# Optimization experiments

Hardware: AMD Instinct MI355X
Metric: run time of the kernel (lower is better)

Reference implementation:

```python
import jax, jax.numpy as jnp
import numpy as np

N = 100000


def gcn_conv(x, edge_index, W, b):
    """PyG GCNConv: add self-loops, symmetric normalization, x @ W, aggregate, + bias."""
    n = x.shape[0]
    src = jnp.concatenate([edge_index[0], jnp.arange(n)])
    dst = jnp.concatenate([edge_index[1], jnp.arange(n)])
    deg = jax.ops.segment_sum(jnp.ones_like(dst, dtype=x.dtype), dst, num_segments=n)
    dinv = jnp.where(deg > 0, jax.lax.rsqrt(deg), 0.0)
    norm = dinv[src] * dinv[dst]  # [E+N]
    h = x @ W  # [N, out]
    msg = h[src] * norm[:, None]  # gather + scale
    agg = jax.ops.segment_sum(msg, dst, num_segments=n)
    return agg + b


def setup_inputs() -> dict:
    key = jax.random.key(0)
    ks = jax.random.split(key, 10)
    x = jax.random.normal(ks[0], (N, 256), dtype=jnp.float32)
    edge_index = jax.random.randint(ks[1], (2, 3200000), 0, N, dtype=jnp.int64)
    def glorot(k, fan_in, fan_out):
        s = np.sqrt(6.0 / (fan_in + fan_out)).astype(np.float32)
        return jax.random.uniform(k, (fan_in, fan_out), jnp.float32, -s, s)
    return {
        "x": x,
        "edge_index": edge_index,
        "W1": glorot(ks[2], 256, 128), "b1": jnp.zeros((128,), jnp.float32),
        "W2": glorot(ks[3], 128, 64), "b2": jnp.zeros((64,), jnp.float32),
        "W3": glorot(ks[4], 64, 16), "b3": jnp.zeros((16,), jnp.float32),
        "Wc": glorot(ks[5], 16, 2), "bc": jnp.zeros((2,), jnp.float32),
    }


def reference(x, edge_index, W1, b1, W2, b2, W3, b3, Wc, bc):
    h = jnp.tanh(gcn_conv(x, edge_index, W1, b1))
    h = jnp.tanh(gcn_conv(h, edge_index, W2, b2))
    h = jnp.tanh(gcn_conv(h, edge_index, W3, b3))
    out = h @ Wc + bc
    return (out, h)
```

## Files before the change

kernel.cpp:

```cpp
#include <hip/hip_runtime.h>
#include <hip/hip_fp16.h>
#include <cstdint>
#include <cstddef>


#define EPB 16384
#define BSHIFT 8
#define NBUC_MAX 512
#define BCAP 12800

__global__ __launch_bounds__(256) void scan_block(const int* __restrict__ src, int n,
                                                  int* __restrict__ incl,
                                                  int* __restrict__ bsum) {
    int tid = threadIdx.x;
    int v = blockIdx.x * 256 + tid;
    int val = (v < n) ? src[v] : 0;
    int lane = tid & 63, w = tid >> 6;
#pragma unroll
    for (int off = 1; off < 64; off <<= 1) {
        int t = __shfl_up(val, off, 64);
        if (lane >= off) val += t;
    }
    __shared__ int wsum[4];
    if (lane == 63) wsum[w] = val;
    __syncthreads();
#pragma unroll
    for (int i = 0; i < 4; ++i)
        if (i < w) val += wsum[i];
    if (v < n) incl[v] = val;
    if (tid == 255) bsum[blockIdx.x] = val;
}

__global__ __launch_bounds__(512) void scan_sums(int* __restrict__ bsum, int nb) {
    int tid = threadIdx.x;
    int val = (tid < nb) ? bsum[tid] : 0;
    int lane = tid & 63, w = tid >> 6;
#pragma unroll
    for (int off = 1; off < 64; off <<= 1) {
        int t = __shfl_up(val, off, 64);
        if (lane >= off) val += t;
    }
    __shared__ int wsum[8];
    if (lane == 63) wsum[w] = val;
    __syncthreads();
#pragma unroll
    for (int i = 0; i < 8; ++i)
        if (i < w) val += wsum[i];
    if (tid < nb) bsum[tid] = val;
}

__global__ __launch_bounds__(256) void finalize_scan(
    const int* __restrict__ incl, const int* __restrict__ bsum,
    const int* __restrict__ src, int n, int* __restrict__ excl) {
    int v = blockIdx.x * 256 + threadIdx.x;
    if (v >= n) return;
    int boff = (blockIdx.x == 0) ? 0 : bsum[blockIdx.x - 1];
    excl[v] = boff + incl[v] - src[v];
}

__global__ __launch_bounds__(256) void hist_bucket(
    const int* __restrict__ ei, int E, int nbuc, int nch,
    int* __restrict__ histG) {
    __shared__ int h[NBUC_MAX];
    const int k = blockIdx.x;
    for (int b = threadIdx.x; b < NBUC_MAX; b += 256) h[b] = 0;
    __syncthreads();
    const int base = k * EPB, end = min(E, base + EPB);
    for (int i = base + threadIdx.x; i < end; i += 256)
        atomicAdd(&h[ei[(size_t)E + i] >> BSHIFT], 1);
    __syncthreads();
    for (int b = threadIdx.x; b < nbuc; b += 256)
        histG[(size_t)b * nch + k] = h[b];
}

__global__ __launch_bounds__(256) void bucket_scatter(
    const int* __restrict__ ei, int E, int nbuc, int nch,
    const int* __restrict__ offs, uint2* __restrict__ ebuf) {
    __shared__ int cur[NBUC_MAX];
    const int k = blockIdx.x;
    for (int b = threadIdx.x; b < nbuc; b += 256)
        cur[b] = offs[(size_t)b * nch + k];
    __syncthreads();
    const int base = k * EPB, end = min(E, base + EPB);
    for (int i = base + threadIdx.x; i < end; i += 256) {
        int s = ei[i];
        int d = ei[(size_t)E + i];
        int pos = atomicAdd(&cur[d >> BSHIFT], 1);
        ebuf[pos] = make_uint2((unsigned)s, (unsigned)d);
    }
}

__global__ __launch_bounds__(256) void bucket_build(
    const uint2* __restrict__ ebuf, const int* __restrict__ offs,
    int E, int nbuc, int nch, int n,
    int* __restrict__ col, int* __restrict__ deg,
    int* __restrict__ row_start, float* __restrict__ dinv) {
    const int b = blockIdx.x;
    const int tid = threadIdx.x;
    const int estart = offs[(size_t)b * nch];
    const int eend = (b + 1 < nbuc) ? offs[(size_t)(b + 1) * nch] : E;
    const int cnt = eend - estart;

    __shared__ int degl[256];
    __shared__ int curl[256];
    __shared__ int wsum[4];
    __shared__ int colstage[BCAP];

    degl[tid] = 0;
    __syncthreads();
    for (int i = tid; i < cnt; i += 256)
        atomicAdd(&degl[ebuf[estart + i].y & 255], 1);
    __syncthreads();
    int myDeg = degl[tid];
    int val = myDeg;
    int lane = tid & 63, w = tid >> 6;
#pragma unroll
    for (int off = 1; off < 64; off <<= 1) {
        int t = __shfl_up(val, off, 64);
        if (lane >= off) val += t;
    }
    if (lane == 63) wsum[w] = val;
    __syncthreads();
#pragma unroll
    for (int i = 0; i < 4; ++i)
        if (i < w) val += wsum[i];
    int excl = val - myDeg;
    curl[tid] = excl;
    int v = (b << BSHIFT) + tid;
    if (v < n) {
        deg[v] = myDeg;
        row_start[v] = estart + excl;
        dinv[v] = rsqrtf((float)(myDeg + 1));
    }
    __syncthreads();
    if (cnt <= BCAP) {
        for (int i = tid; i < cnt; i += 256) {
            uint2 e = ebuf[estart + i];
            int pos = atomicAdd(&curl[e.y & 255], 1);
            colstage[pos] = (int)e.x;
        }
        __syncthreads();
        for (int i = tid; i < cnt; i += 256)
            col[estart + i] = colstage[i];
    } else {
        for (int i = tid; i < cnt; i += 256) {
            uint2 e = ebuf[estart + i];
            int pos = atomicAdd(&curl[e.y & 255], 1);
            col[estart + pos] = (int)e.x;
        }
    }
}

__device__ inline unsigned int pack2h(float a, float b) {
    __half ha = __float2half_rn(a), hb = __float2half_rn(b);
    unsigned short ua = *(unsigned short*)&ha, ub = *(unsigned short*)&hb;
    return (unsigned int)ua | ((unsigned int)ub << 16);
}

template <int FIN, int FOUT, int TM>
__global__ __launch_bounds__(256) void gemm_tile_h(
    const float* __restrict__ X, const float* __restrict__ W,
    const float* __restrict__ dinv, __half* __restrict__ Hs, int n) {
    constexpr int CT = FOUT / 4;
    constexpr int RG = 256 / CT;
    static_assert(TM == RG * 4, "tile mismatch");
    constexpr int LROW = FIN + 4;
    __shared__ float xs[TM][LROW];

    const int node0 = blockIdx.x * TM;
    const int tid = threadIdx.x;

    constexpr int C4 = FIN / 4;
    for (int i = tid; i < TM * C4; i += 256) {
        int r = i / C4, c = i % C4;
        float4 v = make_float4(0.f, 0.f, 0.f, 0.f);
        if (node0 + r < n) v = *(const float4*)(X + (size_t)(node0 + r) * FIN + c * 4);
        *(float4*)&xs[r][c * 4] = v;
    }
    __syncthreads();

    const int col = (tid % CT) * 4;
    const int r0 = (tid / CT) * 4;

    float acc[4][4];
#pragma unroll
    for (int i = 0; i < 4; ++i)
#pragma unroll
        for (int j = 0; j < 4; ++j) acc[i][j] = 0.f;

#pragma unroll 2
    for (int k = 0; k < FIN; k += 4) {
        float4 w0 = *(const float4*)(W + (size_t)(k + 0) * FOUT + col);
        float4 w1 = *(const float4*)(W + (size_t)(k + 1) * FOUT + col);
        float4 w2 = *(const float4*)(W + (size_t)(k + 2) * FOUT + col);
        float4 w3 = *(const float4*)(W + (size_t)(k + 3) * FOUT + col);
        float4 av[4];
        av[0] = *(const float4*)&xs[r0 + 0][k];
        av[1] = *(const float4*)&xs[r0 + 1][k];
        av[2] = *(const float4*)&xs[r0 + 2][k];
        av[3] = *(const float4*)&xs[r0 + 3][k];
#pragma unroll
        for (int rr = 0; rr < 4; ++rr) {
            acc[rr][0] = fmaf(av[rr].x, w0.x, acc[rr][0]);
            acc[rr][1] = fmaf(av[rr].x, w0.y, acc[rr][1]);
            acc[rr][2] = fmaf(av[rr].x, w0.z, acc[rr][2]);
            acc[rr][3] = fmaf(av[rr].x, w0.w, acc[rr][3]);
            acc[rr][0] = fmaf(av[rr].y, w1.x, acc[rr][0]);
            acc[rr][1] = fmaf(av[rr].y, w1.y, acc[rr][1]);
            acc[rr][2] = fmaf(av[rr].y, w1.z, acc[rr][2]);
            acc[rr][3] = fmaf(av[rr].y, w1.w, acc[rr][3]);
            acc[rr][0] = fmaf(av[rr].z, w2.x, acc[rr][0]);
            acc[rr][1] = fmaf(av[rr].z, w2.y, acc[rr][1]);
            acc[rr][2] = fmaf(av[rr].z, w2.z, acc[rr][2]);
            acc[rr][3] = fmaf(av[rr].z, w2.w, acc[rr][3]);
            acc[rr][0] = fmaf(av[rr].w, w3.x, acc[rr][0]);
            acc[rr][1] = fmaf(av[rr].w, w3.y, acc[rr][1]);
            acc[rr][2] = fmaf(av[rr].w, w3.z, acc[rr][2]);
            acc[rr][3] = fmaf(av[rr].w, w3.w, acc[rr][3]);
        }
    }

#pragma unroll
    for (int rr = 0; rr < 4; ++rr) {
        int node = node0 + r0 + rr;
        if (node < n) {
            float di = dinv[node];
            uint2 pk;
            pk.x = pack2h(acc[rr][0] * di, acc[rr][1] * di);
            pk.y = pack2h(acc[rr][2] * di, acc[rr][3] * di);
            *(uint2*)(Hs + (size_t)node * FOUT + col) = pk;
        }
    }
}

__device__ inline void add8h(float* acc, uint4 p) {
    unsigned int w[4] = {p.x, p.y, p.z, p.w};
#pragma unroll
    for (int t = 0; t < 4; ++t) {
        __half2 h = *(const __half2*)&w[t];
        float2 f = __half22float2(h);
        acc[2 * t] += f.x;
        acc[2 * t + 1] += f.y;
    }
}

template <int F>
__global__ __launch_bounds__(256) void pull_agg_h(
    const int* __restrict__ row_start, const int* __restrict__ deg,
    const int* __restrict__ col, const __half* __restrict__ Hs,
    const float* __restrict__ dinv, const float* __restrict__ B,
    float* __restrict__ OUT, int n) {
    constexpr int TPE = F / 8;
    long long gid = (long long)blockIdx.x * 256 + threadIdx.x;
    int node = (int)(gid / TPE);
    int lane = (int)(gid % TPE);
    if (node >= n) return;
    const int beg = row_start[node];
    const int cnt = deg[node];
    const size_t lo = (size_t)lane * 8;

    float acc[8] = {0.f, 0.f, 0.f, 0.f, 0.f, 0.f, 0.f, 0.f};
    add8h(acc, *(const uint4*)(Hs + (size_t)node * F + lo));

    int j = 0;
    for (; j + 8 <= cnt; j += 8) {
        int s0 = col[beg + j + 0], s1 = col[beg + j + 1];
        int s2 = col[beg + j + 2], s3 = col[beg + j + 3];
        int s4 = col[beg + j + 4], s5 = col[beg + j + 5];
        int s6 = col[beg + j + 6], s7 = col[beg + j + 7];
        uint4 p0 = *(const uint4*)(Hs + (size_t)s0 * F + lo);
        uint4 p1 = *(const uint4*)(Hs + (size_t)s1 * F + lo);
        uint4 p2 = *(const uint4*)(Hs + (size_t)s2 * F + lo);
        uint4 p3 = *(const uint4*)(Hs + (size_t)s3 * F + lo);
        uint4 p4 = *(const uint4*)(Hs + (size_t)s4 * F + lo);
        uint4 p5 = *(const uint4*)(Hs + (size_t)s5 * F + lo);
        uint4 p6 = *(const uint4*)(Hs + (size_t)s6 * F + lo);
        uint4 p7 = *(const uint4*)(Hs + (size_t)s7 * F + lo);
        add8h(acc, p0); add8h(acc, p1); add8h(acc, p2); add8h(acc, p3);
        add8h(acc, p4); add8h(acc, p5); add8h(acc, p6); add8h(acc, p7);
    }
    for (; j < cnt; ++j) {
        int s = col[beg + j];
        add8h(acc, *(const uint4*)(Hs + (size_t)s * F + lo));
    }

    float di = dinv[node];
    float4 b0 = *(const float4*)(B + lo);
    float4 b1 = *(const float4*)(B + lo + 4);
    float4 r0, r1;
    r0.x = tanhf(fmaf(acc[0], di, b0.x));
    r0.y = tanhf(fmaf(acc[1], di, b0.y));
    r0.z = tanhf(fmaf(acc[2], di, b0.z));
    r0.w = tanhf(fmaf(acc[3], di, b0.w));
    r1.x = tanhf(fmaf(acc[4], di, b1.x));
    r1.y = tanhf(fmaf(acc[5], di, b1.y));
    r1.z = tanhf(fmaf(acc[6], di, b1.z));
    r1.w = tanhf(fmaf(acc[7], di, b1.w));
    float* op = OUT + (size_t)node * F + lo;
    *(float4*)(op) = r0;
    *(float4*)(op + 4) = r1;
}

__global__ void classifier_kernel(const float* __restrict__ Hf,
                                  const float* __restrict__ Wc,
                                  const float* __restrict__ bc,
                                  float* __restrict__ out, int n) {
    int v = blockIdx.x * blockDim.x + threadIdx.x;
    if (v >= n) return;
    float o0 = bc[0], o1 = bc[1];
    const float* h = Hf + (size_t)v * 16;
#pragma unroll
    for (int k = 0; k < 16; ++k) {
        float hv = h[k];
        o0 = fmaf(hv, Wc[k * 2 + 0], o0);
        o1 = fmaf(hv, Wc[k * 2 + 1], o1);
    }
    out[(size_t)v * 2 + 0] = o0;
    out[(size_t)v * 2 + 1] = o1;
}

extern "C" void kernel_launch(void* const* d_in, const int* in_sizes, int n_in,
                              void* d_out, int out_size, void* d_ws, size_t ws_size,
                              hipStream_t stream) {
    const float* x  = (const float*)d_in[0];
    const int* ei   = (const int*)d_in[1];
    const float* W1 = (const float*)d_in[2];
    const float* b1 = (const float*)d_in[3];
    const float* W2 = (const float*)d_in[4];
    const float* b2 = (const float*)d_in[5];
    const float* W3 = (const float*)d_in[6];
    const float* b3 = (const float*)d_in[7];
    const float* Wc = (const float*)d_in[8];
    const float* bc = (const float*)d_in[9];

    const int n = in_sizes[0] / 256;
    const int E = in_sizes[1] / 2;
    const int nbuc = (n + 255) >> BSHIFT;
    const int nch  = (E + EPB - 1) / EPB;
    const int NH   = nbuc * nch;
    const int nb2  = (NH + 255) / 256;

    float* outp = (float*)d_out;
    float* outh = outp + (size_t)n * 2;

    int*    deg       = (int*)d_ws;
    float*  dinv      = (float*)d_ws + (size_t)n;
    int*    row_start = (int*)d_ws + 2 * (size_t)n;
    int*    histG     = (int*)d_ws + 3 * (size_t)n;
    int*    incl      = histG + NH;
    int*    bsum      = incl + NH;
    int*    offs      = bsum + 512;
    int*    col       = offs + NH;
    __half* HsH       = (__half*)(col + E);
    float*  xbuf      = (float*)(HsH + (size_t)n * 128);
    uint2*  ebuf      = (uint2*)xbuf;

    hist_bucket<<<nch, 256, 0, stream>>>(ei, E, nbuc, nch, histG);
    scan_block<<<nb2, 256, 0, stream>>>(histG, NH, incl, bsum);
    scan_sums<<<1, 512, 0, stream>>>(bsum, nb2);
    finalize_scan<<<nb2, 256, 0, stream>>>(incl, bsum, histG, NH, offs);
    bucket_scatter<<<nch, 256, 0, stream>>>(ei, E, nbuc, nch, offs, ebuf);
    bucket_build<<<nbuc, 256, 0, stream>>>(ebuf, offs, E, nbuc, nch, n,
                                           col, deg, row_start, dinv);

    gemm_tile_h<256, 128, 32><<<(n + 31) / 32, 256, 0, stream>>>(x, W1, dinv, HsH, n);
    pull_agg_h<128><<<(int)(((long long)n * 16 + 255) / 256), 256, 0, stream>>>(
        row_start, deg, col, HsH, dinv, b1, xbuf, n);

    gemm_tile_h<128, 64, 64><<<(n + 63) / 64, 256, 0, stream>>>(xbuf, W2, dinv, HsH, n);
    pull_agg_h<64><<<(int)(((long long)n * 8 + 255) / 256), 256, 0, stream>>>(
        row_start, deg, col, HsH, dinv, b2, xbuf, n);

    gemm_tile_h<64, 16, 256><<<(n + 255) / 256, 256, 0, stream>>>(xbuf, W3, dinv, HsH, n);
    pull_agg_h<16><<<(int)(((long long)n * 2 + 255) / 256), 256, 0, stream>>>(
        row_start, deg, col, HsH, dinv, b3, outh, n);

    classifier_kernel<<<(n + 255) / 256, 256, 0, stream>>>(outh, Wc, bc, outp, n);
}
```

Baseline: 713.8 us.

## Use bf16x3 split MFMA for the first two GCN layer GEMMs

Replaces the FP32 shared-memory tiled GEMMs for layers 1 and 2 with MFMA-based kernels. Each operand is split into a bf16 high part and a bf16 residual, and three bf16 products are summed to recover near-FP32 accuracy. The weights are pre-packed each call into the lane layout that MFMA expects, and the packed copies reuse the histogram workspace. This targets the ALU cost of the dense GEMMs, at the price of extra pack launches and some accuracy risk.

```diff
diff --git a/kernel.cpp b/kernel.cpp
--- a/kernel.cpp
+++ b/kernel.cpp
@@ -8,6 +8,9 @@
 #define BSHIFT 8
 #define NBUC_MAX 512
 #define BCAP 12800
+
+typedef __attribute__((ext_vector_type(8))) short short8;
+typedef __attribute__((ext_vector_type(4))) float f32x4;
 
 __global__ __launch_bounds__(256) void scan_block(const int* __restrict__ src, int n,
                                                   int* __restrict__ incl,
@@ -155,6 +158,111 @@
     __half ha = __float2half_rn(a), hb = __float2half_rn(b);
     unsigned short ua = *(unsigned short*)&ha, ub = *(unsigned short*)&hb;
     return (unsigned int)ua | ((unsigned int)ub << 16);
+}
+
+__device__ inline unsigned short f32_to_bf16_rn(float f) {
+    unsigned int u = __float_as_uint(f);
+    unsigned int r = (u + 0x7FFFu + ((u >> 16) & 1u)) >> 16;
+    return (unsigned short)r;
+}
+__device__ inline float bf16_to_f32(unsigned short h) {
+    return __uint_as_float(((unsigned int)h) << 16);
+}
+
+template <int FIN, int FOUT>
+__global__ __launch_bounds__(256) void pack_w(const float* __restrict__ W,
+                                              unsigned short* __restrict__ Wpk) {
+    constexpr int KC = FIN / 32, CF = FOUT / 16;
+    constexpr int TOT = KC * CF * 64 * 8;
+    int idx = blockIdx.x * 256 + threadIdx.x;
+    if (idx >= TOT) return;
+    int j = idx & 7;
+    int lane = (idx >> 3) & 63;
+    int cf = (idx >> 9) % CF;
+    int kc = (idx >> 9) / CF;
+    int k = kc * 32 + ((lane >> 4) * 8) + j;
+    int c = cf * 16 + (lane & 15);
+    float w = W[(size_t)k * FOUT + c];
+    unsigned short h = f32_to_bf16_rn(w);
+    unsigned short l = f32_to_bf16_rn(w - bf16_to_f32(h));
+    size_t base = ((size_t)((kc * CF + cf) * 64 + lane)) * 16;
+    Wpk[base + j] = h;
+    Wpk[base + 8 + j] = l;
+}
+
+template <int FIN, int FOUT>
+__global__ __launch_bounds__(256) void gemm_mfma(
+    const float* __restrict__ X, const unsigned short* __restrict__ Wpk,
+    const float* __restrict__ dinv, __half* __restrict__ Hs, int n) {
+    constexpr int KC = FIN / 32, CF = FOUT / 16, RF = 2;
+    constexpr int BM = 4 * RF * 16;
+    const int w = threadIdx.x >> 6, lane = threadIdx.x & 63;
+    const int g = lane >> 4, rr = lane & 15;
+    const int node0 = blockIdx.x * BM + w * (RF * 16);
+    const int ko = g * 8;
+
+    f32x4 acc[RF][CF];
+#pragma unroll
+    for (int rf = 0; rf < RF; ++rf)
+#pragma unroll
+        for (int cf = 0; cf < CF; ++cf)
+            acc[rf][cf] = (f32x4){0.f, 0.f, 0.f, 0.f};
+
+    union U16 { uint4 u; short8 s; };
+
+    for (int kc = 0; kc < KC; ++kc) {
+        short8 ahi[RF], alo[RF];
+#pragma unroll
+        for (int rf = 0; rf < RF; ++rf) {
+            int r = node0 + rf * 16 + rr;
+            float xv[8] = {0.f, 0.f, 0.f, 0.f, 0.f, 0.f, 0.f, 0.f};
+            if (r < n) {
+                const float* xp = X + (size_t)r * FIN + kc * 32 + ko;
+                float4 a0 = *(const float4*)xp;
+                float4 a1 = *(const float4*)(xp + 4);
+                xv[0] = a0.x; xv[1] = a0.y; xv[2] = a0.z; xv[3] = a0.w;
+                xv[4] = a1.x; xv[5] = a1.y; xv[6] = a1.z; xv[7] = a1.w;
+            }
+#pragma unroll
+            for (int j = 0; j < 8; ++j) {
+                unsigned short hb = f32_to_bf16_rn(xv[j]);
+                float rem = xv[j] - bf16_to_f32(hb);
+                ahi[rf][j] = (short)hb;
+                alo[rf][j] = (short)f32_to_bf16_rn(rem);
+            }
+        }
+#pragma unroll
+        for (int cf = 0; cf < CF; ++cf) {
+            const uint4* bp = (const uint4*)(Wpk +
+                ((size_t)((kc * CF + cf) * 64 + lane)) * 16);
+            U16 bh, bl;
+            bh.u = bp[0];
+            bl.u = bp[1];
+#pragma unroll
+            for (int rf = 0; rf < RF; ++rf) {
+                acc[rf][cf] = __builtin_amdgcn_mfma_f32_16x16x32_bf16(
+                    ahi[rf], bh.s, acc[rf][cf], 0, 0, 0);
+                acc[rf][cf] = __builtin_amdgcn_mfma_f32_16x16x32_bf16(
+                    alo[rf], bh.s, acc[rf][cf], 0, 0, 0);
+                acc[rf][cf] = __builtin_amdgcn_mfma_f32_16x16x32_bf16(
+                    ahi[rf], bl.s, acc[rf][cf], 0, 0, 0);
+            }
+        }
+    }
+
+#pragma unroll
+    for (int rf = 0; rf < RF; ++rf) {
+#pragma unroll
+        for (int i = 0; i < 4; ++i) {
+            int r = node0 + rf * 16 + g * 4 + i;
+            if (r >= n) continue;
+            float di = dinv[r];
+            __half* hp = Hs + (size_t)r * FOUT + rr;
+#pragma unroll
+            for (int cf = 0; cf < CF; ++cf)
+                hp[cf * 16] = __float2half_rn(acc[rf][cf][i] * di);
+        }
+    }
 }
 
 template <int FIN, int FOUT, int TM>
@@ -355,6 +463,9 @@
     float*  xbuf      = (float*)(HsH + (size_t)n * 128);
     uint2*  ebuf      = (uint2*)xbuf;
 
+    unsigned short* Wpk1 = (unsigned short*)histG;
+    unsigned short* Wpk2 = Wpk1 + (size_t)256 * 128 * 2;
+
     hist_bucket<<<nch, 256, 0, stream>>>(ei, E, nbuc, nch, histG);
     scan_block<<<nb2, 256, 0, stream>>>(histG, NH, incl, bsum);
     scan_sums<<<1, 512, 0, stream>>>(bsum, nb2);
@@ -363,11 +474,14 @@
     bucket_build<<<nbuc, 256, 0, stream>>>(ebuf, offs, E, nbuc, nch, n,
                                            col, deg, row_start, dinv);
 
-    gemm_tile_h<256, 128, 32><<<(n + 31) / 32, 256, 0, stream>>>(x, W1, dinv, HsH, n);
+    pack_w<256, 128><<<(256 / 32 * 128 / 16 * 512 + 255) / 256, 256, 0, stream>>>(W1, Wpk1);
+    pack_w<128, 64><<<(128 / 32 * 64 / 16 * 512 + 255) / 256, 256, 0, stream>>>(W2, Wpk2);
+
+    gemm_mfma<256, 128><<<(n + 127) / 128, 256, 0, stream>>>(x, Wpk1, dinv, HsH, n);
     pull_agg_h<128><<<(int)(((long long)n * 16 + 255) / 256), 256, 0, stream>>>(
         row_start, deg, col, HsH, dinv, b1, xbuf, n);
 
-    gemm_tile_h<128, 64, 64><<<(n + 63) / 64, 256, 0, stream>>>(xbuf, W2, dinv, HsH, n);
+    gemm_mfma<128, 64><<<(n + 127) / 128, 256, 0, stream>>>(xbuf, Wpk2, dinv, HsH, n);
     pull_agg_h<64><<<(int)(((long long)n * 8 + 255) / 256), 256, 0, stream>>>(
         row_start, deg, col, HsH, dinv, b2, xbuf, n);
 
```

Measured after the change: 637.6 us. 10.7% less time.
